# Performance work log

Hardware: AMD Instinct MI355X
Metric: run time of the kernel (lower is better)

## Reference

```python
import jax, jax.numpy as jnp
import numpy as np

SHIFT = 1  # shift_direction fixed to +1 (original picks +/-1 randomly at init)


def setup_inputs() -> dict:
    key = jax.random.key(0)
    k1, k2 = jax.random.split(key)
    x = jax.random.normal(k1, (1, 64, 56, 56), dtype=jnp.float32)
    W = jax.random.normal(k2, (64, 3, 2, 64), dtype=jnp.float32)
    return {"x": x, "W": W}


def reference(x, W):
    # permute 'ijkl -> iljk' and flatten (j,k) -> columns: (1,1,56,3584)
    t2 = jnp.transpose(x, (0, 3, 1, 2)).reshape(1, 1, 56, 3584)
    # unfold kernel (3,1), padding (1,0): three vertically shifted copies with zero pad
    pad = jnp.pad(t2, ((0, 0), (0, 0), (1, 1), (0, 0)))
    taps = jnp.stack([pad[:, 0, t:t + 56, :] for t in range(3)], axis=1)  # (1,3,56,3584)
    taps = taps.reshape(1, 3, 56, 64, 56)  # (m, tap k, o=orig-l, j=channels, n=orig-k)
    # contract taps (k=3) and channels (j=64) against weight (i,k,l,j)
    t3 = jnp.einsum('mkojn,iklj->mioln', taps, W)  # (1,64,56,2,56)
    # merge (o,l)->112, circular roll, split back, sum over the pair dim
    t4 = t3.reshape(1, 64, 112, 56)
    t4 = jnp.roll(t4, SHIFT, axis=2)
    t4 = t4.reshape(1, 64, 56, 2, 56).sum(axis=3)  # (1,64,56,56)
    # final circular roll along last spatial axis
    return jnp.roll(t4, SHIFT, axis=3)
```

## Files before the change

kernel.cpp:

```cpp
#include <hip/hip_runtime.h>

#define SP 56
#define CH 64
#define XSTRIDE 3136

__global__ void tsc_prep(const float* __restrict__ W, float4* __restrict__ Cv) {
  int t = blockIdx.x * blockDim.x + threadIdx.x;
  if (t >= CH * CH) return;
  int i = t & 63;
  int j = t >> 6;
  const float* Wi = W + i * 384 + j;
  float w00 = Wi[0];
  float w01 = Wi[64];
  float w10 = Wi[128];
  float w11 = Wi[192];
  float w20 = Wi[256];
  float w21 = Wi[320];
  Cv[j * 64 + i]        = make_float4(w01, w00 + w11, w10 + w21, w20);
  Cv[4096 + j * 64 + i] = make_float4(w10, w20, w01, w11);
}

__global__ __launch_bounds__(256) void tsc_main(const float* __restrict__ x,
                                                const float4* __restrict__ Cv,
                                                float* __restrict__ out) {
  __shared__ float xs[CH][8];
  __shared__ float red[4][4][64];

  const int t  = threadIdx.x;
  const int i  = t & 63;
  const int w  = t >> 6;
  const int og = blockIdx.x;
  const int n  = blockIdx.y;
  const int o0 = og * 4;
  const int ns = (n + SP - 1) % SP;

  const float* xrow = x + ns * SP;
#pragma unroll
  for (int u = t; u < CH * 8; u += 256) {
    int j = u >> 3;
    int b = u & 7;
    int g = o0 - 2 + b;
    if (g < 0) g += SP;
    float v = (g < SP) ? xrow[j * XSTRIDE + g] : 0.f;
    xs[j][b] = v;
  }
  __syncthreads();

  float a0 = 0.f, a1 = 0.f, a2 = 0.f, a3 = 0.f;
  const float4* cb = Cv + i;
  const int j0 = w * 16;

  if (og != 0) {
#pragma unroll 4
    for (int jj = 0; jj < 16; ++jj) {
      int j = j0 + jj;
      float4 c = cb[j * 64];
      float x0 = xs[j][0], x1 = xs[j][1], x2 = xs[j][2], x3 = xs[j][3];
      float x4 = xs[j][4], x5 = xs[j][5], x6 = xs[j][6];
      a0 += c.x * x0 + c.y * x1 + c.z * x2 + c.w * x3;
      a1 += c.x * x1 + c.y * x2 + c.z * x3 + c.w * x4;
      a2 += c.x * x2 + c.y * x3 + c.z * x4 + c.w * x5;
      a3 += c.x * x3 + c.y * x4 + c.z * x5 + c.w * x6;
    }
  } else {
#pragma unroll 4
    for (int jj = 0; jj < 16; ++jj) {
      int j = j0 + jj;
      float4 c = cb[j * 64];
      float4 d = cb[4096 + j * 64];
      float x0 = xs[j][0], x1 = xs[j][1], x2 = xs[j][2], x3 = xs[j][3];
      float x4 = xs[j][4], x5 = xs[j][5], x6 = xs[j][6];
      a0 += d.x * x2 + d.y * x3 + d.z * x0 + d.w * x1;
      a1 += c.y * x2 + c.z * x3 + c.w * x4;
      a2 += c.x * x2 + c.y * x3 + c.z * x4 + c.w * x5;
      a3 += c.x * x3 + c.y * x4 + c.z * x5 + c.w * x6;
    }
  }

  red[w][0][i] = a0;
  red[w][1][i] = a1;
  red[w][2][i] = a2;
  red[w][3][i] = a3;
  __syncthreads();

  {
    int s  = t >> 6;
    int ii = t & 63;
    float v = red[0][s][ii] + red[1][s][ii] + red[2][s][ii] + red[3][s][ii];
    out[ii * XSTRIDE + (o0 + s) * SP + n] = v;
  }
}

extern "C" void kernel_launch(void* const* d_in, const int* in_sizes, int n_in,
                              void* d_out, int out_size, void* d_ws, size_t ws_size,
                              hipStream_t stream) {
  const float* x = (const float*)d_in[0];
  const float* W = (const float*)d_in[1];
  float* out = (float*)d_out;
  float4* Cv = (float4*)d_ws;

  tsc_prep<<<dim3(16), dim3(256), 0, stream>>>(W, Cv);
  tsc_main<<<dim3(14, 56), dim3(256), 0, stream>>>(x, Cv, out);
}
```

Baseline: 64.83 us.

## Process two output columns per block and preload weights into registers

Each block now computes two adjacent output columns (n0, n0+1), so every weight float4 it loads is reused for both columns, and the grid is halved to 14x28. All 16 weight vectors are prefetched into registers and the x loads are issued before the shared-memory stores, so global latency overlaps. The block count drops to 392 blocks of 256 threads, and register pressure rises from the 16 float4 cache plus 8 accumulators.

```diff
diff --git a/kernel.cpp b/kernel.cpp
--- a/kernel.cpp
+++ b/kernel.cpp
@@ -23,71 +23,104 @@
 __global__ __launch_bounds__(256) void tsc_main(const float* __restrict__ x,
                                                 const float4* __restrict__ Cv,
                                                 float* __restrict__ out) {
-  __shared__ float xs[CH][8];
-  __shared__ float red[4][4][64];
+  __shared__ float xs[2][CH][8];
+  __shared__ float red[4][2][4][64];
 
   const int t  = threadIdx.x;
   const int i  = t & 63;
   const int w  = t >> 6;
   const int og = blockIdx.x;
-  const int n  = blockIdx.y;
+  const int nc = blockIdx.y;
   const int o0 = og * 4;
-  const int ns = (n + SP - 1) % SP;
+  const int n0 = nc * 2;
+  const int ns0 = (n0 + SP - 1) % SP;
+  const int ns1 = n0;
 
-  const float* xrow = x + ns * SP;
+  float xv[4];
 #pragma unroll
-  for (int u = t; u < CH * 8; u += 256) {
-    int j = u >> 3;
+  for (int k = 0; k < 4; ++k) {
+    int u = t + k * 256;
+    int col = u >> 9;
+    int j = (u >> 3) & 63;
     int b = u & 7;
     int g = o0 - 2 + b;
     if (g < 0) g += SP;
-    float v = (g < SP) ? xrow[j * XSTRIDE + g] : 0.f;
-    xs[j][b] = v;
+    int ns = col ? ns1 : ns0;
+    xv[k] = (g < SP) ? x[j * XSTRIDE + ns * SP + g] : 0.f;
+  }
+
+  const float4* cb = Cv + i;
+  const int j0 = w * 16;
+  float4 creg[16];
+#pragma unroll
+  for (int jj = 0; jj < 16; ++jj) creg[jj] = cb[(j0 + jj) * 64];
+
+#pragma unroll
+  for (int k = 0; k < 4; ++k) {
+    int u = t + k * 256;
+    int col = u >> 9;
+    int j = (u >> 3) & 63;
+    int b = u & 7;
+    xs[col][j][b] = xv[k];
   }
   __syncthreads();
 
-  float a0 = 0.f, a1 = 0.f, a2 = 0.f, a3 = 0.f;
-  const float4* cb = Cv + i;
-  const int j0 = w * 16;
+  float a00 = 0.f, a01 = 0.f, a02 = 0.f, a03 = 0.f;
+  float a10 = 0.f, a11 = 0.f, a12 = 0.f, a13 = 0.f;
 
   if (og != 0) {
 #pragma unroll 4
     for (int jj = 0; jj < 16; ++jj) {
       int j = j0 + jj;
-      float4 c = cb[j * 64];
-      float x0 = xs[j][0], x1 = xs[j][1], x2 = xs[j][2], x3 = xs[j][3];
-      float x4 = xs[j][4], x5 = xs[j][5], x6 = xs[j][6];
-      a0 += c.x * x0 + c.y * x1 + c.z * x2 + c.w * x3;
-      a1 += c.x * x1 + c.y * x2 + c.z * x3 + c.w * x4;
-      a2 += c.x * x2 + c.y * x3 + c.z * x4 + c.w * x5;
-      a3 += c.x * x3 + c.y * x4 + c.z * x5 + c.w * x6;
+      float4 c = creg[jj];
+      float x0 = xs[0][j][0], x1 = xs[0][j][1], x2 = xs[0][j][2], x3 = xs[0][j][3];
+      float x4 = xs[0][j][4], x5 = xs[0][j][5], x6 = xs[0][j][6];
+      a00 += c.x * x0 + c.y * x1 + c.z * x2 + c.w * x3;
+      a01 += c.x * x1 + c.y * x2 + c.z * x3 + c.w * x4;
+      a02 += c.x * x2 + c.y * x3 + c.z * x4 + c.w * x5;
+      a03 += c.x * x3 + c.y * x4 + c.z * x5 + c.w * x6;
+      float y0 = xs[1][j][0], y1 = xs[1][j][1], y2 = xs[1][j][2], y3 = xs[1][j][3];
+      float y4 = xs[1][j][4], y5 = xs[1][j][5], y6 = xs[1][j][6];
+      a10 += c.x * y0 + c.y * y1 + c.z * y2 + c.w * y3;
+      a11 += c.x * y1 + c.y * y2 + c.z * y3 + c.w * y4;
+      a12 += c.x * y2 + c.y * y3 + c.z * y4 + c.w * y5;
+      a13 += c.x * y3 + c.y * y4 + c.z * y5 + c.w * y6;
     }
   } else {
 #pragma unroll 4
     for (int jj = 0; jj < 16; ++jj) {
       int j = j0 + jj;
-      float4 c = cb[j * 64];
+      float4 c = creg[jj];
       float4 d = cb[4096 + j * 64];
-      float x0 = xs[j][0], x1 = xs[j][1], x2 = xs[j][2], x3 = xs[j][3];
-      float x4 = xs[j][4], x5 = xs[j][5], x6 = xs[j][6];
-      a0 += d.x * x2 + d.y * x3 + d.z * x0 + d.w * x1;
-      a1 += c.y * x2 + c.z * x3 + c.w * x4;
-      a2 += c.x * x2 + c.y * x3 + c.z * x4 + c.w * x5;
-      a3 += c.x * x3 + c.y * x4 + c.z * x5 + c.w * x6;
+      float x0 = xs[0][j][0], x1 = xs[0][j][1], x2 = xs[0][j][2], x3 = xs[0][j][3];
+      float x4 = xs[0][j][4], x5 = xs[0][j][5], x6 = xs[0][j][6];
+      a00 += d.x * x2 + d.y * x3 + d.z * x0 + d.w * x1;
+      a01 += c.y * x2 + c.z * x3 + c.w * x4;
+      a02 += c.x * x2 + c.y * x3 + c.z * x4 + c.w * x5;
+      a03 += c.x * x3 + c.y * x4 + c.z * x5 + c.w * x6;
+      float y0 = xs[1][j][0], y1 = xs[1][j][1], y2 = xs[1][j][2], y3 = xs[1][j][3];
+      float y4 = xs[1][j][4], y5 = xs[1][j][5], y6 = xs[1][j][6];
+      a10 += d.x * y2 + d.y * y3 + d.z * y0 + d.w * y1;
+      a11 += c.y * y2 + c.z * y3 + c.w * y4;
+      a12 += c.x * y2 + c.y * y3 + c.z * y4 + c.w * y5;
+      a13 += c.x * y3 + c.y * y4 + c.z * y5 + c.w * y6;
     }
   }
 
-  red[w][0][i] = a0;
-  red[w][1][i] = a1;
-  red[w][2][i] = a2;
-  red[w][3][i] = a3;
+  red[w][0][0][i] = a00; red[w][0][1][i] = a01;
+  red[w][0][2][i] = a02; red[w][0][3][i] = a03;
+  red[w][1][0][i] = a10; red[w][1][1][i] = a11;
+  red[w][1][2][i] = a12; red[w][1][3][i] = a13;
   __syncthreads();
 
   {
     int s  = t >> 6;
     int ii = t & 63;
-    float v = red[0][s][ii] + red[1][s][ii] + red[2][s][ii] + red[3][s][ii];
-    out[ii * XSTRIDE + (o0 + s) * SP + n] = v;
+    float v0 = red[0][0][s][ii] + red[1][0][s][ii] + red[2][0][s][ii] + red[3][0][s][ii];
+    float v1 = red[0][1][s][ii] + red[1][1][s][ii] + red[2][1][s][ii] + red[3][1][s][ii];
+    float* ob = out + ii * XSTRIDE + (o0 + s) * SP + n0;
+    ob[0] = v0;
+    ob[1] = v1;
   }
 }
 
@@ -100,5 +133,5 @@
   float4* Cv = (float4*)d_ws;
 
   tsc_prep<<<dim3(16), dim3(256), 0, stream>>>(W, Cv);
-  tsc_main<<<dim3(14, 56), dim3(256), 0, stream>>>(x, Cv, out);
+  tsc_main<<<dim3(14, 28), dim3(256), 0, stream>>>(x, Cv, out);
 }
```

New measurement: 74.34 us. 1.15x slower.
